# Kernel optimization log

Measured on AMD Instinct MI355X. Metric: run time of the kernel, lower is better.

The kernel has to match this reference:

```python
import jax, jax.numpy as jnp
import numpy as np

N_QUBITS = 8
N_LAYERS = 4
DIM = 2 ** N_QUBITS
C64 = jnp.complex64
ROTS = ['RX', 'RY', 'RZ']

# PauliZ sign table: wire 0 is the most-significant bit (PennyLane convention).
_bits = (np.arange(DIM)[:, None] >> (N_QUBITS - 1 - np.arange(N_QUBITS))[None, :]) & 1
Z_SIGNS = jnp.asarray(1.0 - 2.0 * _bits, dtype=jnp.float32)  # (DIM, n_qubits)


def _apply_1q(state, gate, q):
    """Apply a 2x2 gate (or batched (B,2,2) gate) on qubit q. state: (B, DIM) complex64."""
    L = 2 ** q
    R = DIM // (2 * L)
    s = state.reshape(-1, L, 2, R)
    if gate.ndim == 3:
        s = jnp.einsum('bij,bljr->blir', gate, s)
    else:
        s = jnp.einsum('ij,bljr->blir', gate, s)
    return s.reshape(-1, DIM)


def _apply_cnot(state, q):
    """CNOT with control q, target q+1 (adjacent wires): permute basis states."""
    L = 2 ** q
    R = DIM // (4 * L)
    perm = jnp.array([0, 1, 3, 2])
    s = state.reshape(-1, L, 4, R)[:, :, perm, :]
    return s.reshape(-1, DIM)


def _rot(name, t):
    """Scalar-angle single-qubit rotation gate, 2x2 complex64."""
    h = 0.5 * t
    c = jnp.cos(h).astype(C64)
    s = jnp.sin(h).astype(C64)
    if name == 'RX':
        return jnp.stack([jnp.stack([c, -1j * s]), jnp.stack([-1j * s, c])])
    if name == 'RY':
        return jnp.stack([jnp.stack([c, -s]), jnp.stack([s, c])])
    e = jnp.exp(-1j * h).astype(C64)  # RZ = diag(e^{-it/2}, e^{+it/2})
    z = jnp.zeros((), C64)
    return jnp.stack([jnp.stack([e, z]), jnp.stack([z, jnp.conj(e)])])


def _circuit(enc, theta):
    """enc: (B, n_qubits) real angles; theta: (n_layers, n_qubits, 3). Returns <Z_q>: (B, n_qubits)."""
    B = enc.shape[0]
    state = jnp.zeros((B, DIM), C64).at[:, 0].set(1.0)
    # Angle encoding: RY(enc[:, q]) on each wire (batched gate).
    for q in range(N_QUBITS):
        h = 0.5 * enc[:, q]
        c, s = jnp.cos(h), jnp.sin(h)
        g = jnp.stack([jnp.stack([c, -s], -1), jnp.stack([s, c], -1)], -2).astype(C64)
        state = _apply_1q(state, g, q)
    # PCE ansatz: per layer RX/RY/RZ on every qubit, then brickwall CNOT entanglement.
    for l in range(N_LAYERS):
        for q in range(N_QUBITS):
            for r, name in enumerate(ROTS):
                state = _apply_1q(state, _rot(name, theta[l, q, r]), q)
        for i in range(l % 2, N_QUBITS - 1, 2):
            state = _apply_cnot(state, i)
    probs = state.real ** 2 + state.imag ** 2          # (B, DIM)
    return probs @ Z_SIGNS                              # (B, n_qubits)


def setup_inputs() -> dict:
    key = jax.random.key(0)
    k1, k2, k3, k4 = jax.random.split(key, 4)
    B, D_IN, D_OUT = 8192, 512, 512
    x = jax.random.normal(k1, (B, D_IN), dtype=jnp.float32)
    W_in = jax.random.normal(k2, (N_QUBITS, D_IN), dtype=jnp.float32) * (1.0 / np.sqrt(D_IN))
    W_out = jax.random.normal(k3, (D_OUT, N_QUBITS), dtype=jnp.float32) * (1.0 / np.sqrt(N_QUBITS))
    theta = jax.random.normal(k4, (N_LAYERS, N_QUBITS, 3), dtype=jnp.float32) * 0.1
    return {"x": x, "W_in": W_in, "W_out": W_out, "theta": theta}


def reference(x, W_in, W_out, theta):
    enc = jnp.tanh(x @ W_in.T) * jnp.pi     # (B, n_qubits), encoded angles
    z = _circuit(enc, theta)                # (B, n_qubits), PauliZ expvals
    return z @ W_out.T                      # (B, output_dim)
```

## Files before the change

### kernel.cpp

```cpp
#include <hip/hip_runtime.h>
#include <hip/hip_bf16.h>
#include <math.h>


typedef __attribute__((ext_vector_type(8))) short bf16x8;
typedef __attribute__((ext_vector_type(4))) float f32x4;

__device__ __forceinline__ float2 shfl_xor_f2(float2 v, int m) {
  float2 r;
  r.x = __shfl_xor(v.x, m, 64);
  r.y = __shfl_xor(v.y, m, 64);
  return r;
}
__device__ __forceinline__ float2 cfma(float2 u, float2 v, float2 acc) {
  acc.x = fmaf(u.x, v.x, fmaf(-u.y, v.y, acc.x));
  acc.y = fmaf(u.x, v.y, fmaf(u.y, v.x, acc.y));
  return acc;
}

__device__ __forceinline__ void apply_gate(float2 (&a)[4], int q, float2 u00,
                                           float2 u01, float2 u10, float2 u11,
                                           int lane) {
  const float2 z0 = make_float2(0.f, 0.f);
  if (q == 7) {
    float2 n0 = cfma(u00, a[0], cfma(u01, a[1], z0));
    float2 n1 = cfma(u10, a[0], cfma(u11, a[1], z0));
    float2 n2 = cfma(u00, a[2], cfma(u01, a[3], z0));
    float2 n3 = cfma(u10, a[2], cfma(u11, a[3], z0));
    a[0] = n0; a[1] = n1; a[2] = n2; a[3] = n3;
  } else if (q == 6) {
    float2 n0 = cfma(u00, a[0], cfma(u01, a[2], z0));
    float2 n2 = cfma(u10, a[0], cfma(u11, a[2], z0));
    float2 n1 = cfma(u00, a[1], cfma(u01, a[3], z0));
    float2 n3 = cfma(u10, a[1], cfma(u11, a[3], z0));
    a[0] = n0; a[1] = n1; a[2] = n2; a[3] = n3;
  } else {
    int m = 1 << (5 - q);
    bool b = (lane >> (5 - q)) & 1;
    float2 ca = b ? u11 : u00;
    float2 cp = b ? u10 : u01;
    #pragma unroll
    for (int k = 0; k < 4; ++k) {
      float2 p = shfl_xor_f2(a[k], m);
      a[k] = cfma(ca, a[k], cfma(cp, p, z0));
    }
  }
}

__device__ __forceinline__ void apply_cnot(float2 (&a)[4], int q, int lane) {
  if (q <= 4) {
    int m = 1 << (4 - q);
    bool ctrl = (lane >> (5 - q)) & 1;
    #pragma unroll
    for (int k = 0; k < 4; ++k) {
      float2 p = shfl_xor_f2(a[k], m);
      a[k].x = ctrl ? p.x : a[k].x;
      a[k].y = ctrl ? p.y : a[k].y;
    }
  } else if (q == 5) {
    bool ct = lane & 1;
    float2 n0 = ct ? a[2] : a[0];
    float2 n1 = ct ? a[3] : a[1];
    float2 n2 = ct ? a[0] : a[2];
    float2 n3 = ct ? a[1] : a[3];
    a[0] = n0; a[1] = n1; a[2] = n2; a[3] = n3;
  } else {
    float2 t = a[2]; a[2] = a[3]; a[3] = t;
  }
}

__global__ __launch_bounds__(256) void k1_unitary(
    const float* __restrict__ theta, __hip_bfloat16* __restrict__ Bt) {
  __shared__ float mats[32 * 8];
  const int tid = threadIdx.x;
  const int lane = tid & 63;

  if (tid < 32) {
    int l = tid >> 3, q = tid & 7;
    const float* th = theta + (l * 8 + q) * 3;
    float h1 = 0.5f * th[0], h2 = 0.5f * th[1], h3 = 0.5f * th[2];
    float c1 = cosf(h1), s1 = sinf(h1);
    float c2 = cosf(h2), s2 = sinf(h2);
    float c3 = cosf(h3), s3 = sinf(h3);
    float m00r = c2 * c1, m00i = s2 * s1;
    float m01r = -s2 * c1, m01i = -c2 * s1;
    float m10r = s2 * c1, m10i = -c2 * s1;
    float m11r = c1 * c2, m11i = -s1 * s2;
    float* o = &mats[tid * 8];
    o[0] = c3 * m00r + s3 * m00i;  o[1] = c3 * m00i - s3 * m00r;
    o[2] = c3 * m01r + s3 * m01i;  o[3] = c3 * m01i - s3 * m01r;
    o[4] = c3 * m10r - s3 * m10i;  o[5] = c3 * m10i + s3 * m10r;
    o[6] = c3 * m11r - s3 * m11i;  o[7] = c3 * m11i + s3 * m11r;
  }
  __syncthreads();

  const int j = blockIdx.x * 4 + (tid >> 6);
  float2 a[4];
  #pragma unroll
  for (int k = 0; k < 4; ++k)
    a[k] = make_float2((lane * 4 + k == j) ? 1.f : 0.f, 0.f);

  #pragma unroll
  for (int l = 0; l < 4; ++l) {
    #pragma unroll
    for (int q = 0; q < 8; ++q) {
      const float* m = &mats[(l * 8 + q) * 8];
      float2 u00 = make_float2(m[0], m[1]);
      float2 u01 = make_float2(m[2], m[3]);
      float2 u10 = make_float2(m[4], m[5]);
      float2 u11 = make_float2(m[6], m[7]);
      apply_gate(a, q, u00, u01, u10, u11, lane);
    }
    #pragma unroll
    for (int i = (l & 1); i < 7; i += 2) apply_cnot(a, i, lane);
  }
  #pragma unroll
  for (int k = 0; k < 4; ++k) {
    int n0 = (lane * 4 + k) * 2;
    Bt[n0 * 256 + j]       = __float2bfloat16(a[k].x);
    Bt[(n0 + 1) * 256 + j] = __float2bfloat16(a[k].y);
  }
}

__global__ __launch_bounds__(512, 2) void k2_fused(
    const float* __restrict__ x, const float* __restrict__ W_in,
    const float* __restrict__ W_out, const __hip_bfloat16* __restrict__ Bt,
    float* __restrict__ out) {
  __shared__ char psi_lds[32 * 512];
  __shared__ float z_lds[8][32][8];
  __shared__ float z_final[32][8];

  const int tid = threadIdx.x;
  const int lane = tid & 63;
  const int w = tid >> 6;
  const int rowbase = blockIdx.x * 32;

  {
    const float4* W4 = (const float4*)W_in;
    float4 Wa[8], Wb[8];
    #pragma unroll
    for (int q = 0; q < 8; ++q) {
      Wa[q] = W4[q * 128 + lane];
      Wb[q] = W4[q * 128 + 64 + lane];
    }

    #pragma unroll
    for (int rr = 0; rr < 4; ++rr) {
      const int r = w * 4 + rr;
      const float4* x4 = (const float4*)(x + (size_t)(rowbase + r) * 512);
      float4 xa = x4[lane], xb = x4[64 + lane];
      float acc[8];
      #pragma unroll
      for (int q = 0; q < 8; ++q) {
        acc[q] = xa.x * Wa[q].x + xa.y * Wa[q].y + xa.z * Wa[q].z +
                 xa.w * Wa[q].w + xb.x * Wb[q].x + xb.y * Wb[q].y +
                 xb.z * Wb[q].z + xb.w * Wb[q].w;
      }
      #pragma unroll
      for (int m = 1; m < 64; m <<= 1)
        #pragma unroll
        for (int q = 0; q < 8; ++q) acc[q] += __shfl_xor(acc[q], m, 64);

      float cq[8], sq[8];
      #pragma unroll
      for (int q = 0; q < 8; ++q) {
        float e  = __expf(2.f * acc[q]);
        float th = 1.f - __fdividef(2.f, e + 1.f);
        float h  = 1.57079632679489662f * th;
        cq[q] = __cosf(h);
        sq[q] = __sinf(h);
      }
      float base = 1.f;
      #pragma unroll
      for (int q = 0; q < 6; ++q)
        base *= ((lane >> (5 - q)) & 1) ? sq[q] : cq[q];

      __hip_bfloat16 h4[4];
      h4[0] = __float2bfloat16(base * cq[6] * cq[7]);
      h4[1] = __float2bfloat16(base * cq[6] * sq[7]);
      h4[2] = __float2bfloat16(base * sq[6] * cq[7]);
      h4[3] = __float2bfloat16(base * sq[6] * sq[7]);
      int byte = r * 512 + ((lane * 8) ^ ((r & 7) << 4));
      *(uint2*)(psi_lds + byte) = *(uint2*)h4;
    }
  }
  __syncthreads();

  const int cl = lane & 15;
  const int kg = lane >> 4;
  const int wcol = w * 64;

  bf16x8 Af[2][8];
  #pragma unroll
  for (int rt = 0; rt < 2; ++rt)
    #pragma unroll
    for (int kb = 0; kb < 8; ++kb) {
      int row = rt * 16 + cl;
      int byte = row * 512 + ((kg * 16 + kb * 64) ^ ((row & 7) << 4));
      Af[rt][kb] = *(const bf16x8*)(psi_lds + byte);
    }

  f32x4 acc2[2][4];
  #pragma unroll
  for (int rt = 0; rt < 2; ++rt)
    #pragma unroll
    for (int ct = 0; ct < 4; ++ct) acc2[rt][ct] = (f32x4){0.f, 0.f, 0.f, 0.f};

  const short* Bts = (const short*)Bt;
  #pragma unroll
  for (int kb = 0; kb < 8; ++kb) {
    #pragma unroll
    for (int ct = 0; ct < 4; ++ct) {
      bf16x8 bf = *(const bf16x8*)(Bts +
          (size_t)(wcol + ct * 16 + cl) * 256 + kg * 8 + kb * 32);
      acc2[0][ct] = __builtin_amdgcn_mfma_f32_16x16x32_bf16(Af[0][kb], bf,
                                                            acc2[0][ct], 0, 0, 0);
      acc2[1][ct] = __builtin_amdgcn_mfma_f32_16x16x32_bf16(Af[1][kb], bf,
                                                            acc2[1][ct], 0, 0, 0);
    }
  }

  float zacc[2][4][4];
  #pragma unroll
  for (int rt = 0; rt < 2; ++rt)
    #pragma unroll
    for (int u = 0; u < 4; ++u)
      #pragma unroll
      for (int jr = 0; jr < 4; ++jr) zacc[rt][u][jr] = 0.f;

  #pragma unroll
  for (int ct = 0; ct < 4; ++ct) {
    int n = wcol + ct * 16 + cl;
    int i = n >> 1;
    int ib = (lane & 1) ? (i & 15) : (i >> 4);
    float s[4];
    #pragma unroll
    for (int u = 0; u < 4; ++u)
      s[u] = ((ib >> (3 - u)) & 1) ? -1.f : 1.f;
    #pragma unroll
    for (int rt = 0; rt < 2; ++rt) {
      #pragma unroll
      for (int jr = 0; jr < 4; ++jr) {
        float v = acc2[rt][ct][jr];
        v = v * v;
        float P = v + __shfl_xor(v, 1, 64);
        #pragma unroll
        for (int u = 0; u < 4; ++u)
          zacc[rt][u][jr] = fmaf(s[u], P, zacc[rt][u][jr]);
      }
    }
  }

  #pragma unroll
  for (int m = 2; m <= 8; m <<= 1)
    #pragma unroll
    for (int rt = 0; rt < 2; ++rt)
      #pragma unroll
      for (int u = 0; u < 4; ++u)
        #pragma unroll
        for (int jr = 0; jr < 4; ++jr)
          zacc[rt][u][jr] += __shfl_xor(zacc[rt][u][jr], m, 64);

  if (cl <= 1) {
    #pragma unroll
    for (int rt = 0; rt < 2; ++rt)
      #pragma unroll
      for (int u = 0; u < 4; ++u)
        #pragma unroll
        for (int jr = 0; jr < 4; ++jr)
          z_lds[w][rt * 16 + kg * 4 + jr][(lane & 1) * 4 + u] = zacc[rt][u][jr];
  }
  __syncthreads();

  if (tid < 256) {
    int r = tid >> 3, q = tid & 7;
    float s = 0.f;
    #pragma unroll
    for (int wv = 0; wv < 8; ++wv) s += z_lds[wv][r][q];
    z_final[r][q] = s;
  }
  __syncthreads();

  float4 wa = *(const float4*)(W_out + (size_t)tid * 8);
  float4 wb = *(const float4*)(W_out + (size_t)tid * 8 + 4);
  #pragma unroll 4
  for (int r = 0; r < 32; ++r) {
    float4 z0 = *(const float4*)&z_final[r][0];
    float4 z1 = *(const float4*)&z_final[r][4];
    float d = wa.x * z0.x + wa.y * z0.y + wa.z * z0.z + wa.w * z0.w +
              wb.x * z1.x + wb.y * z1.y + wb.z * z1.z + wb.w * z1.w;
    out[(size_t)(rowbase + r) * 512 + tid] = d;
  }
}

extern "C" void kernel_launch(void* const* d_in, const int* in_sizes, int n_in,
                              void* d_out, int out_size, void* d_ws, size_t ws_size,
                              hipStream_t stream) {
  const float* x     = (const float*)d_in[0];
  const float* W_in  = (const float*)d_in[1];
  const float* W_out = (const float*)d_in[2];
  const float* theta = (const float*)d_in[3];
  float* out = (float*)d_out;

  const int B = in_sizes[0] / 512;
  __hip_bfloat16* Bt = (__hip_bfloat16*)d_ws;

  hipLaunchKernelGGL(k1_unitary, dim3(64), dim3(256), 0, stream, theta, Bt);
  hipLaunchKernelGGL(k2_fused, dim3(B / 32), dim3(512), 0, stream,
                     x, W_in, W_out, Bt, out);
}
```

Baseline: 38.58 us.

## Merge unitary and fused kernels into one launch with flag-based synchronisation

```diff
diff --git a/kernel.cpp b/kernel.cpp
--- a/kernel.cpp
+++ b/kernel.cpp
@@ -5,6 +5,19 @@
 
 typedef __attribute__((ext_vector_type(8))) short bf16x8;
 typedef __attribute__((ext_vector_type(4))) float f32x4;
+
+#define MAGIC 0x13572468u
+
+static __device__ __forceinline__ unsigned short f2bf(float f) {
+  __hip_bfloat16 h = __float2bfloat16(f);
+  return *reinterpret_cast<unsigned short*>(&h);
+}
+static __device__ __forceinline__ float bf2f(unsigned short u) {
+  unsigned int v = ((unsigned int)u) << 16;
+  float r;
+  __builtin_memcpy(&r, &v, 4);
+  return r;
+}
 
 __device__ __forceinline__ float2 shfl_xor_f2(float2 v, int m) {
   float2 r;
@@ -69,125 +82,195 @@
   }
 }
 
-__global__ __launch_bounds__(256) void k1_unitary(
-    const float* __restrict__ theta, __hip_bfloat16* __restrict__ Bt) {
-  __shared__ float mats[32 * 8];
-  const int tid = threadIdx.x;
-  const int lane = tid & 63;
-
-  if (tid < 32) {
-    int l = tid >> 3, q = tid & 7;
-    const float* th = theta + (l * 8 + q) * 3;
-    float h1 = 0.5f * th[0], h2 = 0.5f * th[1], h3 = 0.5f * th[2];
-    float c1 = cosf(h1), s1 = sinf(h1);
-    float c2 = cosf(h2), s2 = sinf(h2);
-    float c3 = cosf(h3), s3 = sinf(h3);
-    float m00r = c2 * c1, m00i = s2 * s1;
-    float m01r = -s2 * c1, m01i = -c2 * s1;
-    float m10r = s2 * c1, m10i = -c2 * s1;
-    float m11r = c1 * c2, m11i = -s1 * s2;
-    float* o = &mats[tid * 8];
-    o[0] = c3 * m00r + s3 * m00i;  o[1] = c3 * m00i - s3 * m00r;
-    o[2] = c3 * m01r + s3 * m01i;  o[3] = c3 * m01i - s3 * m01r;
-    o[4] = c3 * m10r - s3 * m10i;  o[5] = c3 * m10i + s3 * m10r;
-    o[6] = c3 * m11r - s3 * m11i;  o[7] = c3 * m11i + s3 * m11r;
-  }
-  __syncthreads();
-
-  const int j = blockIdx.x * 4 + (tid >> 6);
-  float2 a[4];
-  #pragma unroll
-  for (int k = 0; k < 4; ++k)
-    a[k] = make_float2((lane * 4 + k == j) ? 1.f : 0.f, 0.f);
-
-  #pragma unroll
-  for (int l = 0; l < 4; ++l) {
-    #pragma unroll
-    for (int q = 0; q < 8; ++q) {
-      const float* m = &mats[(l * 8 + q) * 8];
-      float2 u00 = make_float2(m[0], m[1]);
-      float2 u01 = make_float2(m[2], m[3]);
-      float2 u10 = make_float2(m[4], m[5]);
-      float2 u11 = make_float2(m[6], m[7]);
-      apply_gate(a, q, u00, u01, u10, u11, lane);
-    }
-    #pragma unroll
-    for (int i = (l & 1); i < 7; i += 2) apply_cnot(a, i, lane);
-  }
-  #pragma unroll
-  for (int k = 0; k < 4; ++k) {
-    int n0 = (lane * 4 + k) * 2;
-    Bt[n0 * 256 + j]       = __float2bfloat16(a[k].x);
-    Bt[(n0 + 1) * 256 + j] = __float2bfloat16(a[k].y);
-  }
-}
-
-__global__ __launch_bounds__(512, 2) void k2_fused(
+__global__ __launch_bounds__(512, 1) void mono_kernel(
     const float* __restrict__ x, const float* __restrict__ W_in,
-    const float* __restrict__ W_out, const __hip_bfloat16* __restrict__ Bt,
+    const float* __restrict__ W_out, const float* __restrict__ theta,
+    __hip_bfloat16* __restrict__ Bt, unsigned* __restrict__ ctrl,
     float* __restrict__ out) {
-  __shared__ char psi_lds[32 * 512];
+  __shared__ float mats[256];
+  __shared__ char Wlds[32768];
+  __shared__ float2 cs_lds[32][8];
+  __shared__ char psi_lds[16384];
   __shared__ float z_lds[8][32][8];
   __shared__ float z_final[32][8];
 
   const int tid = threadIdx.x;
   const int lane = tid & 63;
   const int w = tid >> 6;
-  const int rowbase = blockIdx.x * 32;
+  const int cl = lane & 15;
+  const int kg = lane >> 4;
+  const int bid = blockIdx.x;
+  const int rowbase = bid * 32;
+
+  if (bid < 32) {
+    if (tid < 32) {
+      int l = tid >> 3, q = tid & 7;
+      const float* th = theta + (l * 8 + q) * 3;
+      float h1 = 0.5f * th[0], h2 = 0.5f * th[1], h3 = 0.5f * th[2];
+      float c1 = cosf(h1), s1 = sinf(h1);
+      float c2 = cosf(h2), s2 = sinf(h2);
+      float c3 = cosf(h3), s3 = sinf(h3);
+      float m00r = c2 * c1, m00i = s2 * s1;
+      float m01r = -s2 * c1, m01i = -c2 * s1;
+      float m10r = s2 * c1, m10i = -c2 * s1;
+      float m11r = c1 * c2, m11i = -s1 * s2;
+      float* o = &mats[tid * 8];
+      o[0] = c3 * m00r + s3 * m00i;  o[1] = c3 * m00i - s3 * m00r;
+      o[2] = c3 * m01r + s3 * m01i;  o[3] = c3 * m01i - s3 * m01r;
+      o[4] = c3 * m10r - s3 * m10i;  o[5] = c3 * m10i + s3 * m10r;
+      o[6] = c3 * m11r - s3 * m11i;  o[7] = c3 * m11i + s3 * m11r;
+    }
+    __syncthreads();
+
+    const int j = bid * 8 + w;
+    float2 a[4];
+    #pragma unroll
+    for (int k = 0; k < 4; ++k)
+      a[k] = make_float2((lane * 4 + k == j) ? 1.f : 0.f, 0.f);
+
+    #pragma unroll
+    for (int l = 0; l < 4; ++l) {
+      #pragma unroll
+      for (int q = 0; q < 8; ++q) {
+        const float* m = &mats[(l * 8 + q) * 8];
+        apply_gate(a, q, make_float2(m[0], m[1]), make_float2(m[2], m[3]),
+                   make_float2(m[4], m[5]), make_float2(m[6], m[7]), lane);
+      }
+      #pragma unroll
+      for (int i = (l & 1); i < 7; i += 2) apply_cnot(a, i, lane);
+    }
+    #pragma unroll
+    for (int k = 0; k < 4; ++k) {
+      int n0 = (lane * 4 + k) * 2;
+      Bt[n0 * 256 + j]       = __float2bfloat16(a[k].x);
+      Bt[(n0 + 1) * 256 + j] = __float2bfloat16(a[k].y);
+    }
+    __syncthreads();
+    if (tid == 0) {
+      __threadfence();
+      __hip_atomic_store(&ctrl[bid], MAGIC, __ATOMIC_RELEASE,
+                         __HIP_MEMORY_SCOPE_AGENT);
+    }
+  }
 
   {
-    const float4* W4 = (const float4*)W_in;
-    float4 Wa[8], Wb[8];
-    #pragma unroll
-    for (int q = 0; q < 8; ++q) {
-      Wa[q] = W4[q * 128 + lane];
-      Wb[q] = W4[q * 128 + 64 + lane];
-    }
-
-    #pragma unroll
-    for (int rr = 0; rr < 4; ++rr) {
-      const int r = w * 4 + rr;
-      const float4* x4 = (const float4*)(x + (size_t)(rowbase + r) * 512);
-      float4 xa = x4[lane], xb = x4[64 + lane];
-      float acc[8];
-      #pragma unroll
-      for (int q = 0; q < 8; ++q) {
-        acc[q] = xa.x * Wa[q].x + xa.y * Wa[q].y + xa.z * Wa[q].z +
-                 xa.w * Wa[q].w + xb.x * Wb[q].x + xb.y * Wb[q].y +
-                 xb.z * Wb[q].z + xb.w * Wb[q].w;
+    const int q = tid >> 6;
+    const int ch = tid & 63;
+    float4 wa = *(const float4*)(W_in + q * 512 + ch * 8);
+    float4 wb = *(const float4*)(W_in + q * 512 + ch * 8 + 4);
+    float f[8] = {wa.x, wa.y, wa.z, wa.w, wb.x, wb.y, wb.z, wb.w};
+    unsigned hv[4], lv[4];
+    #pragma unroll
+    for (int i = 0; i < 4; ++i) {
+      unsigned short h0 = f2bf(f[2 * i]), h1 = f2bf(f[2 * i + 1]);
+      unsigned short l0 = f2bf(f[2 * i] - bf2f(h0));
+      unsigned short l1 = f2bf(f[2 * i + 1] - bf2f(h1));
+      hv[i] = (unsigned)h0 | ((unsigned)h1 << 16);
+      lv[i] = (unsigned)l0 | ((unsigned)l1 << 16);
+    }
+    const int swz = (q & 7) << 4;
+    *(uint4*)(Wlds + q * 2048 + ((ch * 16) ^ swz)) =
+        make_uint4(hv[0], hv[1], hv[2], hv[3]);
+    *(uint4*)(Wlds + q * 2048 + ((1024 + ch * 16) ^ swz)) =
+        make_uint4(lv[0], lv[1], lv[2], lv[3]);
+    const int n2 = 8 + (tid >> 6);
+    uint4 z4 = make_uint4(0, 0, 0, 0);
+    *(uint4*)(Wlds + n2 * 2048 + ch * 32) = z4;
+    *(uint4*)(Wlds + n2 * 2048 + ch * 32 + 16) = z4;
+  }
+  __syncthreads();
+
+  if (w < 2) {
+    const int rt = w;
+    const float* xr = x + (size_t)(rowbase + rt * 16 + cl) * 512;
+    f32x4 ea = (f32x4){0.f, 0.f, 0.f, 0.f};
+    const int swz = (cl & 7) << 4;
+    #pragma unroll
+    for (int kb = 0; kb < 16; ++kb) {
+      float4 xa = *(const float4*)(xr + kb * 32 + kg * 8);
+      float4 xb = *(const float4*)(xr + kb * 32 + kg * 8 + 4);
+      float f[8] = {xa.x, xa.y, xa.z, xa.w, xb.x, xb.y, xb.z, xb.w};
+      bf16x8 hi8, lo8;
+      #pragma unroll
+      for (int i = 0; i < 8; ++i) {
+        unsigned short h = f2bf(f[i]);
+        hi8[i] = (short)h;
+        lo8[i] = (short)f2bf(f[i] - bf2f(h));
       }
-      #pragma unroll
-      for (int m = 1; m < 64; m <<= 1)
-        #pragma unroll
-        for (int q = 0; q < 8; ++q) acc[q] += __shfl_xor(acc[q], m, 64);
-
-      float cq[8], sq[8];
-      #pragma unroll
-      for (int q = 0; q < 8; ++q) {
-        float e  = __expf(2.f * acc[q]);
+      bf16x8 bhi = *(const bf16x8*)(Wlds + cl * 2048 +
+                                    ((kg * 16 + kb * 64) ^ swz));
+      bf16x8 blo = *(const bf16x8*)(Wlds + cl * 2048 +
+                                    ((1024 + kg * 16 + kb * 64) ^ swz));
+      ea = __builtin_amdgcn_mfma_f32_16x16x32_bf16(hi8, bhi, ea, 0, 0, 0);
+      ea = __builtin_amdgcn_mfma_f32_16x16x32_bf16(lo8, blo, ea, 0, 0, 0);
+    }
+    if (cl < 8) {
+      #pragma unroll
+      for (int jr = 0; jr < 4; ++jr) {
+        float acc = ea[jr];
+        float e  = __expf(2.f * acc);
         float th = 1.f - __fdividef(2.f, e + 1.f);
         float h  = 1.57079632679489662f * th;
-        cq[q] = __cosf(h);
-        sq[q] = __sinf(h);
+        cs_lds[rt * 16 + kg * 4 + jr][cl] = make_float2(__cosf(h), __sinf(h));
       }
-      float base = 1.f;
-      #pragma unroll
-      for (int q = 0; q < 6; ++q)
-        base *= ((lane >> (5 - q)) & 1) ? sq[q] : cq[q];
-
-      __hip_bfloat16 h4[4];
-      h4[0] = __float2bfloat16(base * cq[6] * cq[7]);
-      h4[1] = __float2bfloat16(base * cq[6] * sq[7]);
-      h4[2] = __float2bfloat16(base * sq[6] * cq[7]);
-      h4[3] = __float2bfloat16(base * sq[6] * sq[7]);
-      int byte = r * 512 + ((lane * 8) ^ ((r & 7) << 4));
-      *(uint2*)(psi_lds + byte) = *(uint2*)h4;
-    }
-  }
-  __syncthreads();
-
-  const int cl = lane & 15;
-  const int kg = lane >> 4;
+    }
+  }
+  __syncthreads();
+
+  {
+    const int row = tid >> 4;
+    const int seg = tid & 15;
+    float2 g0 = cs_lds[row][0], g1 = cs_lds[row][1];
+    float2 g2 = cs_lds[row][2], g3 = cs_lds[row][3];
+    float2 g4 = cs_lds[row][4], g5 = cs_lds[row][5];
+    float2 g6 = cs_lds[row][6], g7 = cs_lds[row][7];
+    float pre = ((seg & 8) ? g0.y : g0.x) * ((seg & 4) ? g1.y : g1.x) *
+                ((seg & 2) ? g2.y : g2.x) * ((seg & 1) ? g3.y : g3.x);
+    float p4[2], p5[4], p6[8], p7[16];
+    p4[0] = pre * g4.x; p4[1] = pre * g4.y;
+    #pragma unroll
+    for (int a = 0; a < 2; ++a) {
+      p5[a * 2]     = p4[a] * g5.x;
+      p5[a * 2 + 1] = p4[a] * g5.y;
+    }
+    #pragma unroll
+    for (int a = 0; a < 4; ++a) {
+      p6[a * 2]     = p5[a] * g6.x;
+      p6[a * 2 + 1] = p5[a] * g6.y;
+    }
+    #pragma unroll
+    for (int a = 0; a < 8; ++a) {
+      p7[a * 2]     = p6[a] * g7.x;
+      p7[a * 2 + 1] = p6[a] * g7.y;
+    }
+    unsigned u[8];
+    #pragma unroll
+    for (int i = 0; i < 8; ++i)
+      u[i] = (unsigned)f2bf(p7[2 * i]) | ((unsigned)f2bf(p7[2 * i + 1]) << 16);
+    const int swz = (row & 7) << 4;
+    *(uint4*)(psi_lds + row * 512 + ((seg * 32) ^ swz)) =
+        make_uint4(u[0], u[1], u[2], u[3]);
+    *(uint4*)(psi_lds + row * 512 + ((seg * 32 + 16) ^ swz)) =
+        make_uint4(u[4], u[5], u[6], u[7]);
+  }
+  __syncthreads();
+
+  if (tid < 32) {
+    while (__hip_atomic_load(&ctrl[tid], __ATOMIC_ACQUIRE,
+                             __HIP_MEMORY_SCOPE_AGENT) != MAGIC)
+      __builtin_amdgcn_s_sleep(2);
+  }
+  __syncthreads();
+  if (tid == 0) {
+    unsigned old = atomicAdd(&ctrl[32], 1u);
+    if (old == 255u || old == 0xAAAAAAAAu + 255u) {
+      #pragma unroll
+      for (int i = 0; i < 33; ++i)
+        __hip_atomic_store(&ctrl[i], 0u, __ATOMIC_RELEASE,
+                           __HIP_MEMORY_SCOPE_AGENT);
+    }
+  }
+
   const int wcol = w * 64;
 
   bf16x8 Af[2][8];
@@ -304,8 +387,8 @@
 
   const int B = in_sizes[0] / 512;
   __hip_bfloat16* Bt = (__hip_bfloat16*)d_ws;
-
-  hipLaunchKernelGGL(k1_unitary, dim3(64), dim3(256), 0, stream, theta, Bt);
-  hipLaunchKernelGGL(k2_fused, dim3(B / 32), dim3(512), 0, stream,
-                     x, W_in, W_out, Bt, out);
-}
+  unsigned* ctrl = (unsigned*)((char*)d_ws + 262144);
+
+  hipLaunchKernelGGL(mono_kernel, dim3(B / 32), dim3(512), 0, stream,
+                     x, W_in, W_out, theta, Bt, ctrl, out);
+}
```

Measured after the change: 86.58 us. +124.4%, slower.
